# Kernel optimization log

Measured on AMD Instinct MI355X. Metric: run time of the kernel, lower is better.

Reference implementation:

```python
import jax, jax.numpy as jnp
import numpy as np

IMG_X, IMG_Y = 1333.0, 402.0   # image_size
MIN_SIZE = 16.0
NMS_THRESH = 0.7
PRE = 12000                    # n_train_pre_nms
POST = 2000                    # n_train_post_nms
HH, WW, A = 83, 25, 9          # 1333//16, 402//16, anchors per cell
N_ANCH = HH * WW * A           # 18675
B = 16


def setup_inputs() -> dict:
    key = jax.random.key(0)
    k1, k2, k3, k4, k5, k6 = jax.random.split(key, 6)
    # realistic anchor boxes inside the image
    xc = jax.random.uniform(k1, (N_ANCH,)) * IMG_X
    yc = jax.random.uniform(k2, (N_ANCH,)) * IMG_Y
    bw = jax.random.uniform(k3, (N_ANCH,)) * 240.0 + 16.0
    bh = jax.random.uniform(k4, (N_ANCH,)) * 120.0 + 16.0
    anchor_boxes = jnp.stack([xc - 0.5 * bw, yc - 0.5 * bh, xc + 0.5 * bw, yc + 0.5 * bh], axis=1)
    rpn_cls_score = jax.random.normal(k5, (B, N_ANCH * 2), dtype=jnp.float32)
    rpn_bbox_pred = jax.random.normal(k6, (B, N_ANCH, 4), dtype=jnp.float32) * 0.2
    return dict(anchor_boxes=anchor_boxes, rpn_cls_score=rpn_cls_score,
                rpn_bbox_pred=rpn_bbox_pred, rpn_cls_loss=jnp.zeros((1,), jnp.float32),
                rpn_bbox_loss=jnp.zeros((1,), jnp.float32))


def _decode(anchor_boxes, rpn_bbox_pred):
    ah = anchor_boxes[:, 3] - anchor_boxes[:, 1]
    aw = anchor_boxes[:, 2] - anchor_boxes[:, 0]
    acy = anchor_boxes[:, 1] + 0.5 * ah
    acx = anchor_boxes[:, 0] + 0.5 * aw
    dx = rpn_bbox_pred[..., 0]
    dy = rpn_bbox_pred[..., 1]
    dw = rpn_bbox_pred[..., 2]
    dh = rpn_bbox_pred[..., 3]
    cy = dy * ah + acy
    cx = dx * aw + acx
    h = jnp.exp(dh) * ah
    w = jnp.exp(dw) * aw
    # clip: x coords to [0, image_size[0]], y coords to [0, image_size[1]] (as in source)
    x1 = jnp.clip(cx - 0.5 * w, 0.0, IMG_X)
    y1 = jnp.clip(cy - 0.5 * h, 0.0, IMG_Y)
    x2 = jnp.clip(cx + 0.5 * w, 0.0, IMG_X)
    y2 = jnp.clip(cy + 0.5 * h, 0.0, IMG_Y)
    return jnp.stack([x1, y1, x2, y2], axis=-1)  # [N,4] broadcast over batch -> [B,N,4]


def _nms_one(roi, score):
    # roi: [N,4], score: [N]
    hs = roi[:, 3] - roi[:, 1]
    ws = roi[:, 2] - roi[:, 0]
    valid = (hs >= MIN_SIZE) & (ws >= MIN_SIZE)
    s = jnp.where(valid, score, -jnp.inf)
    idx = jnp.argsort(-s)[:PRE]          # score-descending, top pre_nms; invalid sink to end
    boxes = roi[idx]                      # score-sorted candidate boxes [PRE,4]
    vp = valid[idx]                       # which slots are real (passed size filter)
    # source quirk: order = order.argsort()[::-1] -> NMS visits boxes by DESCENDING
    # original-anchor-index; invalid slots get key -1 so they come last.
    seq_key = jnp.where(vp, idx, -1)
    perm = jnp.argsort(-seq_key)          # positions into score-sorted arrays, visit order
    x1, y1, x2, y2 = boxes[:, 0], boxes[:, 1], boxes[:, 2], boxes[:, 3]
    areas = (x2 - x1 + 1.0) * (y2 - y1 + 1.0)

    def step(alive, _):
        a_seq = alive[perm]
        any_alive = a_seq.any()
        j = perm[jnp.argmax(a_seq)]       # first surviving box in visit order
        xx1 = jnp.maximum(x1[j], x1)
        yy1 = jnp.maximum(y1[j], y1)
        xx2 = jnp.minimum(x2[j], x2)
        yy2 = jnp.minimum(y2[j], y2)
        inter = jnp.maximum(0.0, xx2 - xx1 + 1.0) * jnp.maximum(0.0, yy2 - yy1 + 1.0)
        ovr = inter / (areas[j] + areas - inter)
        alive = alive & jnp.where(any_alive, ovr <= NMS_THRESH, True)  # j kills itself (ovr=1)
        return alive, jnp.where(any_alive, j, -1)

    _, keep = jax.lax.scan(step, vp, None, length=POST)   # up to post_nms kept positions
    kmask = keep >= 0
    out = jnp.where(kmask[:, None], boxes[jnp.maximum(keep, 0)], 0.0)  # padded [POST,4]
    return out, kmask


def reference(anchor_boxes, rpn_cls_score, rpn_bbox_pred, rpn_cls_loss, rpn_bbox_loss):
    bsz = rpn_cls_score.shape[0]
    # objectness = view(B, 83, 25, 9, 2)[..., 1]
    score = rpn_cls_score.reshape(bsz, HH, WW, A, 2)[..., 1].reshape(bsz, -1)
    roi = _decode(anchor_boxes, rpn_bbox_pred)            # [B,N,4]
    rois, mask = jax.vmap(_nms_one)(roi, score)           # [B,POST,4], [B,POST]
    return rois, mask
```

## Files before the change

kernel.cpp:

```cpp
#include <hip/hip_runtime.h>
#include <math.h>

#define N_ANCHN 18675
#define NPAD    18688
#define BATCH   16
#define PRE     12000
#define CPAD    12032
#define WPB     188
#define POST    2000
#define NMS_T   0.7f
#define IMGX    1333.0f
#define IMGY    402.0f
#define MINSZ   16.0f
#define NBUCK   256
#define KINV    0x007FFFFFu
#define MLCAP   12288

typedef unsigned long long u64;

__device__ __forceinline__ unsigned key_of(float f) {
  unsigned u = __float_as_uint(f);
  return (u & 0x80000000u) ? ~u : (u | 0x80000000u);
}

__device__ __forceinline__ float iou_ref(float ax1, float ay1, float ax2, float ay2, float aar,
                                         float bx1, float by1, float bx2, float by2, float bar) {
  float xx1 = fmaxf(ax1, bx1);
  float yy1 = fmaxf(ay1, by1);
  float xx2 = fminf(ax2, bx2);
  float yy2 = fminf(ay2, by2);
  float iw = fmaxf(0.0f, __fadd_rn(__fsub_rn(xx2, xx1), 1.0f));
  float ih = fmaxf(0.0f, __fadd_rn(__fsub_rn(yy2, yy1), 1.0f));
  float inter = __fmul_rn(iw, ih);
  return __fdiv_rn(inter, __fsub_rn(__fadd_rn(aar, bar), inter));
}

__device__ __forceinline__ bool hit_test(float ix1, float iy1, float ix2, float iy2, float iar,
                                         float jx1, float jy1, float jx2, float jy2, float jar) {
  float xx1 = fmaxf(ix1, jx1);
  float yy1 = fmaxf(iy1, jy1);
  float xx2 = fminf(ix2, jx2);
  float yy2 = fminf(iy2, jy2);
  float iw = fmaxf(0.0f, __fadd_rn(__fsub_rn(xx2, xx1), 1.0f));
  float ih = fmaxf(0.0f, __fadd_rn(__fsub_rn(yy2, yy1), 1.0f));
  float inter = __fmul_rn(iw, ih);
  float S = __fadd_rn(iar, jar);
  if (inter >= __fmul_rn(0.43f, S)) return true;
  if (inter <= __fmul_rn(0.395f, S)) return false;
  return __fdiv_rn(inter, __fsub_rn(S, inter)) > NMS_T;
}

__device__ __forceinline__ void emit_hit(int lo, int hi, u64* diagb, unsigned* rcb,
                                         unsigned short* rtb, int L) {
  if ((hi >> 6) == (lo >> 6)) {
    atomicOr(&diagb[(size_t)(lo >> 6) * 64 + (lo & 63)], 1ull << (hi & 63));
  } else {
    unsigned slot = atomicAdd(&rcb[lo], 1u);
    if ((int)slot < L) rtb[(size_t)lo * L + slot] = (unsigned short)hi;
  }
}

__device__ __forceinline__ void decode_one(
    const float* __restrict__ anchors, const float* __restrict__ cls,
    const float* __restrict__ bbox, int b, int i,
    float& x1, float& y1, float& x2, float& y2, unsigned& key) {
  float4 A = *(const float4*)(anchors + (size_t)i * 4);
  float ah = __fsub_rn(A.w, A.y);
  float aw = __fsub_rn(A.z, A.x);
  float acy = __fadd_rn(A.y, __fmul_rn(0.5f, ah));
  float acx = __fadd_rn(A.x, __fmul_rn(0.5f, aw));

  float4 P = *(const float4*)(bbox + ((size_t)b * N_ANCHN + i) * 4);
  float dx = P.x, dy = P.y, dw = P.z, dh = P.w;

  float cy = __fadd_rn(__fmul_rn(dy, ah), acy);
  float cx = __fadd_rn(__fmul_rn(dx, aw), acx);
  float eh = (float)exp((double)dh);
  float ew = (float)exp((double)dw);
  float h = __fmul_rn(eh, ah);
  float w = __fmul_rn(ew, aw);

  x1 = fminf(fmaxf(__fsub_rn(cx, __fmul_rn(0.5f, w)), 0.0f), IMGX);
  y1 = fminf(fmaxf(__fsub_rn(cy, __fmul_rn(0.5f, h)), 0.0f), IMGY);
  x2 = fminf(fmaxf(__fadd_rn(cx, __fmul_rn(0.5f, w)), 0.0f), IMGX);
  y2 = fminf(fmaxf(__fadd_rn(cy, __fmul_rn(0.5f, h)), 0.0f), IMGY);

  bool valid = (__fsub_rn(y2, y1) >= MINSZ) && (__fsub_rn(x2, x1) >= MINSZ);
  float s = valid ? cls[(size_t)b * (2 * N_ANCHN) + 2 * i + 1] : -INFINITY;
  key = key_of(s);
}

__global__ __launch_bounds__(256) void decode_kernel(
    const float* __restrict__ anchors, const float* __restrict__ cls,
    const float* __restrict__ bbox,
    float* __restrict__ bx1, float* __restrict__ by1,
    float* __restrict__ bx2, float* __restrict__ by2,
    unsigned* __restrict__ keys,
    u64* __restrict__ diag, unsigned* __restrict__ rowcnt) {
  const int bx = blockIdx.x;
  const int b = blockIdx.y;
  if (bx == gridDim.x - 1) {
    u64* dz = diag + (size_t)b * WPB * 64;
    for (int i = threadIdx.x; i < WPB * 64; i += 256) dz[i] = 0ull;
    unsigned* rz = rowcnt + (size_t)b * CPAD;
    for (int i = threadIdx.x; i < CPAD; i += 256) rz[i] = 0u;
    return;
  }
  int i = bx * 256 + threadIdx.x;
  if (i >= N_ANCHN) return;
  float x1, y1, x2, y2; unsigned k;
  decode_one(anchors, cls, bbox, b, i, x1, y1, x2, y2, k);
  size_t o = (size_t)b * NPAD + i;
  bx1[o] = x1; by1[o] = y1; bx2[o] = x2; by2[o] = y2;
  keys[o] = k;
}

__global__ __launch_bounds__(1024) void prepsort_kernel(
    const unsigned* __restrict__ keys,
    const float* __restrict__ bx1, const float* __restrict__ by1,
    const float* __restrict__ bx2, const float* __restrict__ by2,
    float* __restrict__ cx1, float* __restrict__ cy1,
    float* __restrict__ cx2, float* __restrict__ cy2,
    float* __restrict__ car, int* __restrict__ ncand,
    float* __restrict__ sx1, float* __restrict__ sy1,
    float* __restrict__ sx2, float* __restrict__ sy2,
    float* __restrict__ sar, int* __restrict__ sperm,
    float* __restrict__ wminx1, float* __restrict__ wmaxx2) {
  const int b = blockIdx.x;
  const int tid = threadIdx.x;
  const int lane = tid & 63;
  const int wv = tid >> 6;
  __shared__ unsigned hist[16][256];
  __shared__ unsigned mh[256];
  __shared__ unsigned wsum[16];
  __shared__ unsigned bh[NBUCK];
  __shared__ unsigned boff[NBUCK];
  __shared__ unsigned char fb[NPAD];
  __shared__ unsigned short mlist[MLCAP];
  __shared__ unsigned sh_prefix, sh_k, sh_n, sh_mcount;
  const unsigned* kb = keys + (size_t)b * NPAD;

  if (tid == 0) { sh_prefix = 0u; sh_k = PRE; sh_mcount = 0u; }
  __syncthreads();

  {
    for (int idx = tid; idx < 16 * 256; idx += 1024) ((unsigned*)hist)[idx] = 0u;
    __syncthreads();
    for (int i = tid; i < N_ANCHN; i += 1024)
      atomicAdd(&hist[wv][kb[i] >> 24], 1u);
    __syncthreads();
    if (tid < 256) {
      unsigned s = 0;
#pragma unroll
      for (int q = 0; q < 16; ++q) s += hist[q][tid];
      mh[tid] = s;
    }
    __syncthreads();
    if (tid == 0) {
      unsigned kk = sh_k, cum = 0;
      for (int d = 255; d >= 0; --d) {
        unsigned c = mh[d];
        if (cum + c >= kk) { sh_k = kk - cum; sh_prefix = (unsigned)d << 24; break; }
        cum += c;
      }
    }
    __syncthreads();
  }

  {
    unsigned b0 = sh_prefix >> 24;
    for (int i = tid; i < N_ANCHN; i += 1024) {
      if ((kb[i] >> 24) == b0) {
        unsigned p = atomicAdd(&sh_mcount, 1u);
        if (p < MLCAP) mlist[p] = (unsigned short)i;
      }
    }
  }
  __syncthreads();
  const bool useList = (sh_mcount <= (unsigned)MLCAP);
  const unsigned mcount = min(sh_mcount, (unsigned)MLCAP);

  for (int level = 1; level < 4; ++level) {
    const int shift = 24 - 8 * level;
    for (int idx = tid; idx < 16 * 256; idx += 1024) ((unsigned*)hist)[idx] = 0u;
    __syncthreads();
    unsigned pre = sh_prefix;
    if (useList) {
      for (int idx = tid; idx < (int)mcount; idx += 1024) {
        unsigned k = kb[mlist[idx]];
        if ((k >> (shift + 8)) == (pre >> (shift + 8)))
          atomicAdd(&hist[wv][(k >> shift) & 255u], 1u);
      }
    } else {
      for (int i = tid; i < N_ANCHN; i += 1024) {
        unsigned k = kb[i];
        if ((k >> (shift + 8)) == (pre >> (shift + 8)))
          atomicAdd(&hist[wv][(k >> shift) & 255u], 1u);
      }
    }
    __syncthreads();
    if (tid < 256) {
      unsigned s = 0;
#pragma unroll
      for (int q = 0; q < 16; ++q) s += hist[q][tid];
      mh[tid] = s;
    }
    __syncthreads();
    if (tid == 0) {
      unsigned kk = sh_k, cum = 0;
      for (int d = 255; d >= 0; --d) {
        unsigned c = mh[d];
        if (cum + c >= kk) { sh_k = kk - cum; sh_prefix = pre | ((unsigned)d << shift); break; }
        cum += c;
      }
    }
    __syncthreads();
  }
  const unsigned T = sh_prefix;
  const unsigned slots = sh_k;

  const int SEG = (N_ANCHN + 1023) / 1024;

  {
    int i0 = tid * SEG, i1 = min(N_ANCHN, i0 + SEG);
    unsigned cnt = 0;
    for (int i = i0; i < i1; ++i) cnt += (kb[i] == T) ? 1u : 0u;
    unsigned v = cnt;
#pragma unroll
    for (int d = 1; d < 64; d <<= 1) {
      unsigned y = __shfl_up(v, d, 64);
      if (lane >= d) v += y;
    }
    if (lane == 63) wsum[wv] = v;
    __syncthreads();
    if (tid == 0) {
      unsigned acc = 0;
#pragma unroll
      for (int q = 0; q < 16; ++q) { unsigned t = wsum[q]; wsum[q] = acc; acc += t; }
    }
    __syncthreads();
    unsigned r = wsum[wv] + v - cnt;
    for (int i = i0; i < i1; ++i) {
      unsigned k = kb[i];
      bool tie = (k == T);
      bool cand = (k > T) || (tie && T > KINV && r < slots);
      if (tie) r++;
      fb[i] = cand ? (unsigned char)1 : (unsigned char)0;
    }
  }
  __syncthreads();

  const float* X1 = bx1 + (size_t)b * NPAD;
  const float* Y1 = by1 + (size_t)b * NPAD;
  const float* X2 = bx2 + (size_t)b * NPAD;
  const float* Y2 = by2 + (size_t)b * NPAD;
  {
    int j0 = tid * SEG, j1 = min(N_ANCHN, j0 + SEG);
    unsigned cnt = 0;
    for (int j = j0; j < j1; ++j) cnt += fb[N_ANCHN - 1 - j];
    unsigned v = cnt;
#pragma unroll
    for (int d = 1; d < 64; d <<= 1) {
      unsigned y = __shfl_up(v, d, 64);
      if (lane >= d) v += y;
    }
    if (lane == 63) wsum[wv] = v;
    __syncthreads();
    if (tid == 0) {
      unsigned acc = 0;
#pragma unroll
      for (int q = 0; q < 16; ++q) { unsigned t = wsum[q]; wsum[q] = acc; acc += t; }
      sh_n = acc;
    }
    __syncthreads();
    unsigned p = wsum[wv] + v - cnt;
    if (tid == 0) ncand[b] = (int)sh_n;
    float* CX1 = cx1 + (size_t)b * CPAD;
    float* CY1 = cy1 + (size_t)b * CPAD;
    float* CX2 = cx2 + (size_t)b * CPAD;
    float* CY2 = cy2 + (size_t)b * CPAD;
    float* CAR = car + (size_t)b * CPAD;
    for (int j = j0; j < j1; ++j) {
      int i = N_ANCHN - 1 - j;
      if (fb[i]) {
        float x1v = X1[i], y1v = Y1[i], x2v = X2[i], y2v = Y2[i];
        CX1[p] = x1v; CY1[p] = y1v; CX2[p] = x2v; CY2[p] = y2v;
        CAR[p] = __fmul_rn(__fadd_rn(__fsub_rn(x2v, x1v), 1.0f),
                           __fadd_rn(__fsub_rn(y2v, y1v), 1.0f));
        p++;
      }
    }
  }
  __syncthreads();
  const int n = (int)sh_n;

  const float scale = (float)NBUCK / 1334.0f;
  const float* CX1 = cx1 + (size_t)b * CPAD;
  const float* CY1 = cy1 + (size_t)b * CPAD;
  const float* CX2 = cx2 + (size_t)b * CPAD;
  const float* CY2 = cy2 + (size_t)b * CPAD;
  const float* CAR = car + (size_t)b * CPAD;
  float* SX1 = sx1 + (size_t)b * CPAD;
  float* SY1 = sy1 + (size_t)b * CPAD;
  float* SX2 = sx2 + (size_t)b * CPAD;
  float* SY2 = sy2 + (size_t)b * CPAD;
  float* SAR = sar + (size_t)b * CPAD;
  int* SP = sperm + (size_t)b * CPAD;

  if (tid < NBUCK) bh[tid] = 0u;
  __syncthreads();
  for (int i = tid; i < n; i += 1024) {
    int q = (int)(CX1[i] * scale);
    q = q < 0 ? 0 : (q > NBUCK - 1 ? NBUCK - 1 : q);
    atomicAdd(&bh[q], 1u);
  }
  __syncthreads();
  if (tid < 64) {
    unsigned carry = 0;
    for (int c = 0; c < 4; ++c) {
      unsigned own = bh[c * 64 + tid];
      unsigned v = own;
      for (int d = 1; d < 64; d <<= 1) {
        unsigned y = __shfl_up(v, d, 64);
        if (tid >= d) v += y;
      }
      boff[c * 64 + tid] = carry + v - own;
      carry += __shfl(v, 63, 64);
    }
  }
  __syncthreads();
  for (int i = tid; i < n; i += 1024) {
    float x1v = CX1[i];
    int q = (int)(x1v * scale);
    q = q < 0 ? 0 : (q > NBUCK - 1 ? NBUCK - 1 : q);
    unsigned p = atomicAdd(&boff[q], 1u);
    SX1[p] = x1v; SY1[p] = CY1[i]; SX2[p] = CX2[i]; SY2[p] = CY2[i];
    SAR[p] = CAR[i]; SP[p] = i;
  }
  for (int i = n + tid; i < CPAD; i += 1024) {
    SX1[i] = 1e30f; SY1[i] = 1e30f; SX2[i] = -1e30f; SY2[i] = -1e30f;
    SAR[i] = 1.0f; SP[i] = 0;
  }
  __syncthreads();
  for (int w = wv; w < WPB; w += 16) {
    float mn = SX1[64 * w + lane];
    float mx = SX2[64 * w + lane];
#pragma unroll
    for (int d = 32; d > 0; d >>= 1) {
      mn = fminf(mn, __shfl_xor(mn, d, 64));
      mx = fmaxf(mx, __shfl_xor(mx, d, 64));
    }
    if (lane == 0) {
      wminx1[(size_t)b * WPB + w] = mn;
      wmaxx2[(size_t)b * WPB + w] = mx;
    }
  }
}

__global__ __launch_bounds__(256) void build_kernel(
    const float* __restrict__ sx1, const float* __restrict__ sy1,
    const float* __restrict__ sx2, const float* __restrict__ sy2,
    const float* __restrict__ sar, const int* __restrict__ sperm,
    const int* __restrict__ ncand,
    const float* __restrict__ wminx1, const float* __restrict__ wmaxx2,
    u64* __restrict__ diagT, unsigned* __restrict__ rowcnt,
    unsigned short* __restrict__ rows_t, int L) {
  const int R = blockIdx.x, G0 = blockIdx.y, b = blockIdx.z;
  const int n = ncand[b];
  if (64 * R >= n) return;
  if (16 * G0 + 15 < R) return;
  const float* WMN = wminx1 + (size_t)b * WPB;
  const float rlim = __fadd_rn(wmaxx2[(size_t)b * WPB + R], 2.0f);
  {
    const int wlo = max(16 * G0, R);
    if (WMN[wlo] > __fadd_rn(rlim, 5.25f)) return;
  }

  const float* SX1 = sx1 + (size_t)b * CPAD;
  const float* SY1 = sy1 + (size_t)b * CPAD;
  const float* SX2 = sx2 + (size_t)b * CPAD;
  const float* SY2 = sy2 + (size_t)b * CPAD;
  const float* SAR = sar + (size_t)b * CPAD;
  const int* SP = sperm + (size_t)b * CPAD;

  const int t = threadIdx.x, lane = t & 63, q = t >> 6;

  __shared__ float4 rbv[64];
  __shared__ float2 ras[64];
  if (t < 64) {
    int i = 64 * R + t;
    rbv[t] = make_float4(SX1[i], SY1[i], SX2[i], SY2[i]);
  } else if (t < 128) {
    int i = 64 * R + (t - 64);
    ras[t - 64] = make_float2(SAR[i], __int_as_float(SP[i]));
  }
  const float rx2own = SX2[64 * R + lane];
  __syncthreads();

  const int w0 = 16 * G0 + 4 * q;
  const float wmn0 = WMN[min(w0 + 0, WPB - 1)];
  const float wmn1 = WMN[min(w0 + 1, WPB - 1)];
  const float wmn2 = WMN[min(w0 + 2, WPB - 1)];
  const float wmn3 = WMN[min(w0 + 3, WPB - 1)];
  const bool v0 = (w0 + 0 < WPB) && (w0 + 0 >= R) && (wmn0 <= rlim);
  const bool v1 = (w0 + 1 < WPB) && (w0 + 1 >= R) && (wmn1 <= rlim);
  const bool v2 = (w0 + 2 < WPB) && (w0 + 2 >= R) && (wmn2 <= rlim);
  const bool v3 = (w0 + 3 < WPB) && (w0 + 3 >= R) && (wmn3 <= rlim);
  if (!(v0 | v1 | v2 | v3)) return;

  float c0x1 = 1e30f, c0y1 = 0.f, c0x2 = 0.f, c0y2 = 0.f, c0ar = 1.f; int c0sp = 0;
  float c1x1 = 1e30f, c1y1 = 0.f, c1x2 = 0.f, c1y2 = 0.f, c1ar = 1.f; int c1sp = 0;
  float c2x1 = 1e30f, c2y1 = 0.f, c2x2 = 0.f, c2y2 = 0.f, c2ar = 1.f; int c2sp = 0;
  float c3x1 = 1e30f, c3y1 = 0.f, c3x2 = 0.f, c3y2 = 0.f, c3ar = 1.f; int c3sp = 0;
  if (v0) { int j = 64 * (w0 + 0) + lane;
    c0x1 = SX1[j]; c0y1 = SY1[j]; c0x2 = SX2[j]; c0y2 = SY2[j]; c0ar = SAR[j]; c0sp = SP[j]; }
  if (v1) { int j = 64 * (w0 + 1) + lane;
    c1x1 = SX1[j]; c1y1 = SY1[j]; c1x2 = SX2[j]; c1y2 = SY2[j]; c1ar = SAR[j]; c1sp = SP[j]; }
  if (v2) { int j = 64 * (w0 + 2) + lane;
    c2x1 = SX1[j]; c2y1 = SY1[j]; c2x2 = SX2[j]; c2y2 = SY2[j]; c2ar = SAR[j]; c2sp = SP[j]; }
  if (v3) { int j = 64 * (w0 + 3) + lane;
    c3x1 = SX1[j]; c3y1 = SY1[j]; c3x2 = SX2[j]; c3y2 = SY2[j]; c3ar = SAR[j]; c3sp = SP[j]; }

  const float wmnlo = v0 ? wmn0 : (v1 ? wmn1 : (v2 ? wmn2 : wmn3));
  u64 a = __ballot(rx2own >= __fsub_rn(wmnlo, 2.0f));
  if (!a) return;

  const float wmn0m2 = __fsub_rn(wmn0, 2.0f);
  const float wmn1m2 = __fsub_rn(wmn1, 2.0f);
  const float wmn2m2 = __fsub_rn(wmn2, 2.0f);
  const float wmn3m2 = __fsub_rn(wmn3, 2.0f);

  u64* diagb = diagT + (size_t)b * WPB * 64;
  unsigned* rcb = rowcnt + (size_t)b * CPAD;
  unsigned short* rtb = rows_t + (size_t)b * L * CPAD;

  const bool diagIn = (w0 <= R) & (R <= w0 + 3);
  if (!diagIn) {
    int k = (int)__builtin_ctzll(a);
    float4 RB = rbv[k];
    float2 AS = ras[k];
    while (true) {
      a &= a - 1;
      const int kn = a ? (int)__builtin_ctzll(a) : 0;
      const float4 RBn = rbv[kn];
      const float2 ASn = ras[kn];
      const float rx2k = RB.z;
      const float rark = AS.x;
      const int rsp = __float_as_int(AS.y);
      if (v0 && rx2k >= wmn0m2 &&
          hit_test(RB.x, RB.y, RB.z, RB.w, rark, c0x1, c0y1, c0x2, c0y2, c0ar))
        emit_hit(min(rsp, c0sp), max(rsp, c0sp), diagb, rcb, rtb, L);
      if (v1 && rx2k >= wmn1m2 &&
          hit_test(RB.x, RB.y, RB.z, RB.w, rark, c1x1, c1y1, c1x2, c1y2, c1ar))
        emit_hit(min(rsp, c1sp), max(rsp, c1sp), diagb, rcb, rtb, L);
      if (v2 && rx2k >= wmn2m2 &&
          hit_test(RB.x, RB.y, RB.z, RB.w, rark, c2x1, c2y1, c2x2, c2y2, c2ar))
        emit_hit(min(rsp, c2sp), max(rsp, c2sp), diagb, rcb, rtb, L);
      if (v3 && rx2k >= wmn3m2 &&
          hit_test(RB.x, RB.y, RB.z, RB.w, rark, c3x1, c3y1, c3x2, c3y2, c3ar))
        emit_hit(min(rsp, c3sp), max(rsp, c3sp), diagb, rcb, rtb, L);
      if (!a) break;
      RB = RBn; AS = ASn;
    }
  } else {
    const bool g0 = (w0 + 0 > R), e0 = (w0 + 0 == R);
    const bool g1 = (w0 + 1 > R), e1 = (w0 + 1 == R);
    const bool g2 = (w0 + 2 > R), e2 = (w0 + 2 == R);
    const bool g3 = (w0 + 3 > R), e3 = (w0 + 3 == R);
    int k = (int)__builtin_ctzll(a);
    float4 RB = rbv[k];
    float2 AS = ras[k];
    while (true) {
      a &= a - 1;
      const int kn = a ? (int)__builtin_ctzll(a) : 0;
      const float4 RBn = rbv[kn];
      const float2 ASn = ras[kn];
      const float rx2k = RB.z;
      const float rark = AS.x;
      const int rsp = __float_as_int(AS.y);
      if (v0 && rx2k >= wmn0m2) {
        bool dd = g0 | (e0 & (lane > k));
        if (dd && hit_test(RB.x, RB.y, RB.z, RB.w, rark, c0x1, c0y1, c0x2, c0y2, c0ar))
          emit_hit(min(rsp, c0sp), max(rsp, c0sp), diagb, rcb, rtb, L);
      }
      if (v1 && rx2k >= wmn1m2) {
        bool dd = g1 | (e1 & (lane > k));
        if (dd && hit_test(RB.x, RB.y, RB.z, RB.w, rark, c1x1, c1y1, c1x2, c1y2, c1ar))
          emit_hit(min(rsp, c1sp), max(rsp, c1sp), diagb, rcb, rtb, L);
      }
      if (v2 && rx2k >= wmn2m2) {
        bool dd = g2 | (e2 & (lane > k));
        if (dd && hit_test(RB.x, RB.y, RB.z, RB.w, rark, c2x1, c2y1, c2x2, c2y2, c2ar))
          emit_hit(min(rsp, c2sp), max(rsp, c2sp), diagb, rcb, rtb, L);
      }
      if (v3 && rx2k >= wmn3m2) {
        bool dd = g3 | (e3 & (lane > k));
        if (dd && hit_test(RB.x, RB.y, RB.z, RB.w, rark, c3x1, c3y1, c3x2, c3y2, c3ar))
          emit_hit(min(rsp, c3sp), max(rsp, c3sp), diagb, rcb, rtb, L);
      }
      if (!a) break;
      k = kn; RB = RBn; AS = ASn;
    }
  }
}

#define DECLW(s) u64 kw##s; unsigned cw##s; uint4 p0##s, p1##s;
#define LOADW(s, wexp) { int w_ = (wexp); int c_ = 64 * w_ + lane; \
  kw##s = diagb[(size_t)w_ * 64 + lane]; cw##s = rcb[c_]; \
  const uint4* rp_ = (const uint4*)(rtb + (size_t)c_ * L); p0##s = rp_[0]; p1##s = rp_[1]; }
#define PROCW(s, wexp) { int w_ = (wexp); \
  if (w_ < nw && sc < POST) { \
    const int base_ = 64 * w_; const int myc_ = base_ + lane; \
    const u64 suppw_ = supp[w_]; \
    const bool alv_ = (myc_ < n) && !((suppw_ >> lane) & 1ull); \
    u64 act_ = __ballot(alv_); \
    u64 selw_ = 0ull; \
    const int scb_ = sc; \
    const unsigned klo_ = (unsigned)kw##s, khi_ = (unsigned)(kw##s >> 32); \
    while (act_ && sc < POST) { \
      const int j_ = (int)__builtin_ctzll(act_); \
      const u64 kj_ = ((u64)(unsigned)__builtin_amdgcn_readlane((int)khi_, j_) << 32) | \
                      (u64)(unsigned)__builtin_amdgcn_readlane((int)klo_, j_); \
      selw_ |= 1ull << j_; sc++; \
      act_ &= ~(kj_ | (1ull << j_)); } \
    const bool selme_ = ((selw_ >> lane) & 1ull) != 0ull; \
    if (selme_) { \
      const int rank_ = scb_ + (int)__popcll(selw_ & ((1ull << lane) - 1ull)); \
      sel[rank_] = myc_; \
      const int ce_ = min((int)cw##s, L); \
      uint4 p2_ = {0,0,0,0}, p3_ = {0,0,0,0}; \
      if (ce_ > 16) { \
        const uint4* rp_ = (const uint4*)(rtb + (size_t)myc_ * L); \
        p2_ = rp_[2]; p3_ = rp_[3]; \
      } \
      unsigned ev_[8] = {p0##s.x, p0##s.y, p0##s.z, p0##s.w, p1##s.x, p1##s.y, p1##s.z, p1##s.w}; \
      _Pragma("unroll") \
      for (int u_ = 0; u_ < 8; ++u_) { \
        if (2 * u_ < ce_)     { int t_ = (int)(ev_[u_] & 0xffffu); atomicOr(&supp[t_ >> 6], 1ull << (t_ & 63)); } \
        if (2 * u_ + 1 < ce_) { int t_ = (int)(ev_[u_] >> 16);     atomicOr(&supp[t_ >> 6], 1ull << (t_ & 63)); } } \
      if (ce_ > 16) { \
        unsigned e2_[8] = {p2_.x, p2_.y, p2_.z, p2_.w, p3_.x, p3_.y, p3_.z, p3_.w}; \
        _Pragma("unroll") \
        for (int u_ = 0; u_ < 8; ++u_) { \
          if (16 + 2 * u_ < ce_)     { int t_ = (int)(e2_[u_] & 0xffffu); atomicOr(&supp[t_ >> 6], 1ull << (t_ & 63)); } \
          if (16 + 2 * u_ + 1 < ce_) { int t_ = (int)(e2_[u_] >> 16);     atomicOr(&supp[t_ >> 6], 1ull << (t_ & 63)); } } } } \
    u64 om_ = __ballot(selme_ && ((int)cw##s > L)); \
    while (om_) { \
      int j_ = (int)__builtin_ctzll(om_); om_ &= om_ - 1; \
      const int mc_ = base_ + j_; \
      float ax1_ = CX1[mc_], ay1_ = CY1[mc_], ax2_ = CX2[mc_], ay2_ = CY2[mc_], aar_ = CAR[mc_]; \
      for (int c2_ = base_ + 64 + lane; c2_ < n; c2_ += 64) { \
        float ovr_ = iou_ref(ax1_, ay1_, ax2_, ay2_, aar_, CX1[c2_], CY1[c2_], CX2[c2_], CY2[c2_], CAR[c2_]); \
        if (ovr_ > NMS_T) atomicOr(&supp[c2_ >> 6], 1ull << (c2_ & 63)); } } } }

#define LOADG(s, gexp) { int g_ = (gexp); \
  LOADW(s##0, min(4 * g_ + 0, WPB - 1)) \
  LOADW(s##1, min(4 * g_ + 1, WPB - 1)) \
  LOADW(s##2, min(4 * g_ + 2, WPB - 1)) \
  LOADW(s##3, min(4 * g_ + 3, WPB - 1)) }
#define PROCG(s, gexp) { int gg_ = (gexp); \
  PROCW(s##0, 4 * gg_ + 0) \
  PROCW(s##1, 4 * gg_ + 1) \
  PROCW(s##2, 4 * gg_ + 2) \
  PROCW(s##3, 4 * gg_ + 3) }

__global__ __launch_bounds__(64) void scan_kernel(
    const float* __restrict__ cx1, const float* __restrict__ cy1,
    const float* __restrict__ cx2, const float* __restrict__ cy2,
    const float* __restrict__ car, const int* __restrict__ ncand,
    const u64* __restrict__ diagT, const unsigned* __restrict__ rowcnt,
    const unsigned short* __restrict__ rows_t, int L,
    float* __restrict__ out) {
  const int b = blockIdx.x;
  const int lane = threadIdx.x;
  __shared__ u64 supp[WPB];
  __shared__ int sel[POST];
  for (int idx = lane; idx < WPB; idx += 64) supp[idx] = 0ull;

  const int n = ncand[b];
  const u64* diagb = diagT + (size_t)b * WPB * 64;
  const unsigned* rcb = rowcnt + (size_t)b * CPAD;
  const unsigned short* rtb = rows_t + (size_t)b * L * CPAD;
  const float* CX1 = cx1 + (size_t)b * CPAD;
  const float* CY1 = cy1 + (size_t)b * CPAD;
  const float* CX2 = cx2 + (size_t)b * CPAD;
  const float* CY2 = cy2 + (size_t)b * CPAD;
  const float* CAR = car + (size_t)b * CPAD;

  const int nw = (n + 63) >> 6;
  int sc = 0;

  DECLW(a0) DECLW(a1) DECLW(a2) DECLW(a3)
  DECLW(b0) DECLW(b1) DECLW(b2) DECLW(b3)
  DECLW(c0) DECLW(c1) DECLW(c2) DECLW(c3)

  if (nw > 0) {
    LOADG(a, 0)
    LOADG(b, 1)
    LOADG(c, 2)
    const int ng = (nw + 3) >> 2;
    for (int g = 0; g < ng && sc < POST; g += 3) {
      PROCG(a, g)
      LOADG(a, g + 3)
      PROCG(b, g + 1)
      LOADG(b, g + 4)
      PROCG(c, g + 2)
      LOADG(c, g + 5)
    }
  }

  float* roib = out + (size_t)b * POST * 4;
  float* maskb = out + (size_t)BATCH * POST * 4 + (size_t)b * POST;
  for (int t = lane; t < POST; t += 64) {
    if (t < sc) {
      int j = sel[t];
      float4 v = make_float4(CX1[j], CY1[j], CX2[j], CY2[j]);
      *(float4*)(roib + (size_t)t * 4) = v;
      maskb[t] = 1.0f;
    } else {
      *(float4*)(roib + (size_t)t * 4) = make_float4(0.f, 0.f, 0.f, 0.f);
      maskb[t] = 0.0f;
    }
  }
}

__global__ __launch_bounds__(256) void decode_fb_kernel(
    const float* __restrict__ anchors, const float* __restrict__ cls,
    const float* __restrict__ bbox,
    float* __restrict__ bx1, float* __restrict__ by1,
    float* __restrict__ bx2, float* __restrict__ by2,
    unsigned* __restrict__ keys) {
  int i = blockIdx.x * 256 + threadIdx.x;
  if (i >= N_ANCHN) return;
  int b = blockIdx.y;
  float x1, y1, x2, y2; unsigned k;
  decode_one(anchors, cls, bbox, b, i, x1, y1, x2, y2, k);
  size_t o = (size_t)b * NPAD + i;
  bx1[o] = x1; by1[o] = y1; bx2[o] = x2; by2[o] = y2;
  keys[o] = k;
}

__global__ __launch_bounds__(1024) void prep_kernel(
    const unsigned* __restrict__ keys,
    const float* __restrict__ bx1, const float* __restrict__ by1,
    const float* __restrict__ bx2, const float* __restrict__ by2,
    unsigned char* __restrict__ flags,
    float* __restrict__ cx1, float* __restrict__ cy1,
    float* __restrict__ cx2, float* __restrict__ cy2,
    float* __restrict__ car, int* __restrict__ ncand) {
  const int b = blockIdx.x;
  const int tid = threadIdx.x;
  __shared__ unsigned hist[256];
  __shared__ unsigned ssc[1024];
  __shared__ unsigned sh_prefix, sh_k;
  const unsigned* kb = keys + (size_t)b * NPAD;

  if (tid == 0) { sh_prefix = 0u; sh_k = PRE; }
  __syncthreads();

  for (int level = 0; level < 4; ++level) {
    const int shift = 24 - 8 * level;
    if (tid < 256) hist[tid] = 0u;
    __syncthreads();
    unsigned pre = sh_prefix;
    for (int i = tid; i < N_ANCHN; i += 1024) {
      unsigned k = kb[i];
      bool match = (level == 0) || ((k >> (shift + 8)) == (pre >> (shift + 8)));
      if (match) atomicAdd(&hist[(k >> shift) & 255u], 1u);
    }
    __syncthreads();
    if (tid == 0) {
      unsigned kk = sh_k, cum = 0;
      for (int d = 255; d >= 0; --d) {
        unsigned c = hist[d];
        if (cum + c >= kk) { sh_k = kk - cum; sh_prefix = pre | ((unsigned)d << shift); break; }
        cum += c;
      }
    }
    __syncthreads();
  }
  const unsigned T = sh_prefix;

  unsigned local = 0;
  for (int i = tid; i < N_ANCHN; i += 1024) local += (kb[i] > T) ? 1u : 0u;
  ssc[tid] = local;
  __syncthreads();
  for (int off = 512; off > 0; off >>= 1) {
    if (tid < off) ssc[tid] += ssc[tid + off];
    __syncthreads();
  }
  const unsigned slots = PRE - ssc[0];
  __syncthreads();

  const int SEG = (N_ANCHN + 1023) / 1024;
  const float* X1 = bx1 + (size_t)b * NPAD;
  const float* Y1 = by1 + (size_t)b * NPAD;
  const float* X2 = bx2 + (size_t)b * NPAD;
  const float* Y2 = by2 + (size_t)b * NPAD;
  unsigned char* fb = flags + (size_t)b * NPAD;

  {
    int i0 = tid * SEG, i1 = min(N_ANCHN, i0 + SEG);
    unsigned cnt = 0;
    for (int i = i0; i < i1; ++i) cnt += (kb[i] == T) ? 1u : 0u;
    ssc[tid] = cnt;
    __syncthreads();
    for (int off = 1; off < 1024; off <<= 1) {
      unsigned v = (tid >= off) ? ssc[tid - off] : 0u;
      __syncthreads();
      ssc[tid] += v;
      __syncthreads();
    }
    unsigned r = ssc[tid] - cnt;
    for (int i = i0; i < i1; ++i) {
      unsigned k = kb[i];
      bool valid = (__fsub_rn(Y2[i], Y1[i]) >= MINSZ) && (__fsub_rn(X2[i], X1[i]) >= MINSZ);
      bool tie = (k == T);
      bool cand = valid && ((k > T) || (tie && r < slots));
      if (tie) r++;
      fb[i] = cand ? (unsigned char)1 : (unsigned char)0;
    }
  }
  __syncthreads();

  {
    int j0 = tid * SEG, j1 = min(N_ANCHN, j0 + SEG);
    unsigned cnt = 0;
    for (int j = j0; j < j1; ++j) cnt += fb[N_ANCHN - 1 - j];
    ssc[tid] = cnt;
    __syncthreads();
    for (int off = 1; off < 1024; off <<= 1) {
      unsigned v = (tid >= off) ? ssc[tid - off] : 0u;
      __syncthreads();
      ssc[tid] += v;
      __syncthreads();
    }
    unsigned p = ssc[tid] - cnt;
    if (tid == 0) ncand[b] = (int)ssc[1023];
    float* CX1 = cx1 + (size_t)b * CPAD;
    float* CY1 = cy1 + (size_t)b * CPAD;
    float* CX2 = cx2 + (size_t)b * CPAD;
    float* CY2 = cy2 + (size_t)b * CPAD;
    float* CAR = car + (size_t)b * CPAD;
    for (int j = j0; j < j1; ++j) {
      int i = N_ANCHN - 1 - j;
      if (fb[i]) {
        float x1v = X1[i], y1v = Y1[i], x2v = X2[i], y2v = Y2[i];
        CX1[p] = x1v; CY1[p] = y1v; CX2[p] = x2v; CY2[p] = y2v;
        CAR[p] = __fmul_rn(__fadd_rn(__fsub_rn(x2v, x1v), 1.0f),
                           __fadd_rn(__fsub_rn(y2v, y1v), 1.0f));
        p++;
      }
    }
  }
}

__global__ __launch_bounds__(1024) void nms_kernel(
    const float* __restrict__ cx1, const float* __restrict__ cy1,
    const float* __restrict__ cx2, const float* __restrict__ cy2,
    const float* __restrict__ car, const int* __restrict__ ncand,
    float* __restrict__ out) {
  const int b = blockIdx.x;
  const int tid = threadIdx.x;
  __shared__ float sx1[POST], sy1[POST], sx2[POST], sy2[POST], sar[POST];
  __shared__ int Lbuf[1024];
  __shared__ int wcount[16];
  __shared__ int sh_sc;

  const float* CX1 = cx1 + (size_t)b * CPAD;
  const float* CY1 = cy1 + (size_t)b * CPAD;
  const float* CX2 = cx2 + (size_t)b * CPAD;
  const float* CY2 = cy2 + (size_t)b * CPAD;
  const float* CAR = car + (size_t)b * CPAD;
  float* roib = out + (size_t)b * POST * 4;
  float* maskb = out + (size_t)BATCH * POST * 4 + (size_t)b * POST;

  const int n = ncand[b];
  if (tid == 0) sh_sc = 0;
  __syncthreads();
  const int lane = tid & 63;
  const int w = tid >> 6;

  for (int base = 0; base < n; base += 1024) {
    const int c = base + tid;
    bool pass = (c < n);
    float px1 = 0, py1 = 0, px2 = 0, py2 = 0, par = 0;
    if (pass) { px1 = CX1[c]; py1 = CY1[c]; px2 = CX2[c]; py2 = CY2[c]; par = CAR[c]; }
    const int sc0 = sh_sc;

    if (pass) {
      for (int k = 0; k < sc0; ++k) {
        float ovr = iou_ref(sx1[k], sy1[k], sx2[k], sy2[k], sar[k], px1, py1, px2, py2, par);
        if (ovr > NMS_T) { pass = false; break; }
      }
    }

    unsigned long long bal = __ballot(pass);
    if (lane == 0) wcount[w] = (int)__popcll(bal);
    __syncthreads();
    int off = 0;
    for (int q = 0; q < 16; ++q) off += (q < w) ? wcount[q] : 0;
    if (pass) Lbuf[off + (int)__popcll(bal & ((1ULL << lane) - 1ULL))] = c;
    __syncthreads();

    if (tid < 64) {
      int total = 0;
      for (int q = 0; q < 16; ++q) total += wcount[q];
      int sc = sc0;
      for (int g = 0; g < total && sc < POST; g += 64) {
        int idx = (g + lane < total) ? Lbuf[g + lane] : -1;
        float qx1 = 0, qy1 = 0, qx2 = 0, qy2 = 0, qar = 0;
        bool al = (idx >= 0);
        if (al) { qx1 = CX1[idx]; qy1 = CY1[idx]; qx2 = CX2[idx]; qy2 = CY2[idx]; qar = CAR[idx]; }
        for (int k = sc0; k < sc && al; ++k) {
          float ovr = iou_ref(sx1[k], sy1[k], sx2[k], sy2[k], sar[k], qx1, qy1, qx2, qy2, qar);
          if (ovr > NMS_T) al = false;
        }
        unsigned long long alive = __ballot(al);
        while (alive && sc < POST) {
          int j = (int)__builtin_ctzll(alive);
          float jx1 = __shfl(qx1, j), jy1 = __shfl(qy1, j);
          float jx2 = __shfl(qx2, j), jy2 = __shfl(qy2, j), jar = __shfl(qar, j);
          float ovr = iou_ref(jx1, jy1, jx2, jy2, jar, qx1, qy1, qx2, qy2, qar);
          unsigned long long killm = __ballot(ovr > NMS_T);
          alive &= ~killm;
          alive &= ~(1ULL << j);
          if (lane == 0) {
            sx1[sc] = jx1; sy1[sc] = jy1; sx2[sc] = jx2; sy2[sc] = jy2; sar[sc] = jar;
            roib[(size_t)sc * 4 + 0] = jx1;
            roib[(size_t)sc * 4 + 1] = jy1;
            roib[(size_t)sc * 4 + 2] = jx2;
            roib[(size_t)sc * 4 + 3] = jy2;
          }
          sc++;
        }
      }
      if (lane == 0) sh_sc = sc;
    }
    __syncthreads();
    if (sh_sc >= POST) break;
  }
  __syncthreads();

  const int sc = sh_sc;
  for (int t = tid; t < POST; t += 1024) {
    if (t >= sc) {
      roib[(size_t)t * 4 + 0] = 0.f; roib[(size_t)t * 4 + 1] = 0.f;
      roib[(size_t)t * 4 + 2] = 0.f; roib[(size_t)t * 4 + 3] = 0.f;
    }
    maskb[t] = (t < sc) ? 1.0f : 0.0f;
  }
}

extern "C" void kernel_launch(void* const* d_in, const int* in_sizes, int n_in,
                              void* d_out, int out_size, void* d_ws, size_t ws_size,
                              hipStream_t stream) {
  const float* anchors = (const float*)d_in[0];
  const float* cls = (const float*)d_in[1];
  const float* bbox = (const float*)d_in[2];
  float* out = (float*)d_out;
  char* ws = (char*)d_ws;

  size_t o = 0;
  float* cx1 = (float*)(ws + o); o += (size_t)BATCH * CPAD * 4;
  float* cy1 = (float*)(ws + o); o += (size_t)BATCH * CPAD * 4;
  float* cx2 = (float*)(ws + o); o += (size_t)BATCH * CPAD * 4;
  float* cy2 = (float*)(ws + o); o += (size_t)BATCH * CPAD * 4;
  float* car = (float*)(ws + o); o += (size_t)BATCH * CPAD * 4;
  int* ncand = (int*)(ws + o); o += 256;
  u64* diag = (u64*)(ws + o); o += (size_t)BATCH * WPB * 64 * 8;
  unsigned* rowcnt = (unsigned*)(ws + o); o += (size_t)BATCH * CPAD * 4;
  float* wminx1 = (float*)(ws + o); o += (size_t)BATCH * WPB * 4;
  float* wmaxx2 = (float*)(ws + o); o += (size_t)BATCH * WPB * 4;
  float* sx1 = (float*)(ws + o); o += (size_t)BATCH * CPAD * 4;
  float* sy1 = (float*)(ws + o); o += (size_t)BATCH * CPAD * 4;
  float* sx2 = (float*)(ws + o); o += (size_t)BATCH * CPAD * 4;
  float* sy2 = (float*)(ws + o); o += (size_t)BATCH * CPAD * 4;
  float* sar = (float*)(ws + o); o += (size_t)BATCH * CPAD * 4;
  int* sperm = (int*)(ws + o); o += (size_t)BATCH * CPAD * 4;
  size_t overlay = o;
  unsigned* keys = (unsigned*)(ws + overlay);
  float* bx1 = (float*)(ws + overlay + (size_t)BATCH * NPAD * 4 * 1);
  float* by1 = (float*)(ws + overlay + (size_t)BATCH * NPAD * 4 * 2);
  float* bx2 = (float*)(ws + overlay + (size_t)BATCH * NPAD * 4 * 3);
  float* by2 = (float*)(ws + overlay + (size_t)BATCH * NPAD * 4 * 4);
  size_t decode_bytes = (size_t)BATCH * NPAD * 4 * 5;
  unsigned short* rows_t = (unsigned short*)(ws + overlay);

  int L = 0;
  for (int Ltry = 32; Ltry >= 16; Ltry -= 16) {
    size_t rows_bytes = (size_t)BATCH * Ltry * CPAD * 2;
    size_t need = overlay + (decode_bytes > rows_bytes ? decode_bytes : rows_bytes);
    if (ws_size >= need) { L = Ltry; break; }
  }

  if (L > 0) {
    dim3 dgrid((N_ANCHN + 255) / 256 + 1, BATCH);
    decode_kernel<<<dgrid, 256, 0, stream>>>(anchors, cls, bbox, bx1, by1, bx2, by2,
                                             keys, diag, rowcnt);
    prepsort_kernel<<<BATCH, 1024, 0, stream>>>(keys, bx1, by1, bx2, by2,
                                                cx1, cy1, cx2, cy2, car, ncand,
                                                sx1, sy1, sx2, sy2, sar, sperm,
                                                wminx1, wmaxx2);
    build_kernel<<<dim3(WPB, (WPB + 15) / 16, BATCH), 256, 0, stream>>>(
        sx1, sy1, sx2, sy2, sar, sperm, ncand, wminx1, wmaxx2,
        diag, rowcnt, rows_t, L);
    scan_kernel<<<BATCH, 64, 0, stream>>>(cx1, cy1, cx2, cy2, car, ncand,
                                          diag, rowcnt, rows_t, L, out);
  } else {
    size_t f = 0;
    unsigned* fkeys = (unsigned*)(ws + f); f += (size_t)BATCH * NPAD * 4;
    float* fbx1 = (float*)(ws + f); f += (size_t)BATCH * NPAD * 4;
    float* fby1 = (float*)(ws + f); f += (size_t)BATCH * NPAD * 4;
    float* fbx2 = (float*)(ws + f); f += (size_t)BATCH * NPAD * 4;
    float* fby2 = (float*)(ws + f); f += (size_t)BATCH * NPAD * 4;
    float* fcx1 = (float*)(ws + f); f += (size_t)BATCH * CPAD * 4;
    float* fcy1 = (float*)(ws + f); f += (size_t)BATCH * CPAD * 4;
    float* fcx2 = (float*)(ws + f); f += (size_t)BATCH * CPAD * 4;
    float* fcy2 = (float*)(ws + f); f += (size_t)BATCH * CPAD * 4;
    float* fcar = (float*)(ws + f); f += (size_t)BATCH * CPAD * 4;
    unsigned char* fflags = (unsigned char*)(ws + f); f += (size_t)BATCH * NPAD;
    int* fncand = (int*)(ws + f); f += 256;

    dim3 dgrid((N_ANCHN + 255) / 256, BATCH);
    decode_fb_kernel<<<dgrid, 256, 0, stream>>>(anchors, cls, bbox, fbx1, fby1, fbx2, fby2, fkeys);
    prep_kernel<<<BATCH, 1024, 0, stream>>>(fkeys, fbx1, fby1, fbx2, fby2, fflags,
                                            fcx1, fcy1, fcx2, fcy2, fcar, fncand);
    nms_kernel<<<BATCH, 1024, 0, stream>>>(fcx1, fcy1, fcx2, fcy2, fcar, fncand, out);
  }
}
```

Before: 530.1 us.

## Use x-sorted window pruning for overflow rows and allow larger per-row lists

In the scan kernel, a selected box whose suppression list overflows the stored row length no longer compares against every later candidate by brute force. It walks the x-sorted candidate copy and uses per-word min/max x bounds to skip or stop early, then maps hits back through the permutation. The stored row length can now reach 64 entries, with a tail loop reading entries past 32, so fewer rows overflow. In exchange this uses more workspace and memory traffic for the row table, and adds some serial per-entry atomics.

```diff
diff --git a/kernel.cpp b/kernel.cpp
--- a/kernel.cpp
+++ b/kernel.cpp
@@ -543,15 +543,25 @@
         _Pragma("unroll") \
         for (int u_ = 0; u_ < 8; ++u_) { \
           if (16 + 2 * u_ < ce_)     { int t_ = (int)(e2_[u_] & 0xffffu); atomicOr(&supp[t_ >> 6], 1ull << (t_ & 63)); } \
-          if (16 + 2 * u_ + 1 < ce_) { int t_ = (int)(e2_[u_] >> 16);     atomicOr(&supp[t_ >> 6], 1ull << (t_ & 63)); } } } } \
+          if (16 + 2 * u_ + 1 < ce_) { int t_ = (int)(e2_[u_] >> 16);     atomicOr(&supp[t_ >> 6], 1ull << (t_ & 63)); } } } \
+      for (int e_ = 32; e_ < ce_; ++e_) { \
+        int t_ = (int)rtb[(size_t)myc_ * L + e_]; atomicOr(&supp[t_ >> 6], 1ull << (t_ & 63)); } } \
     u64 om_ = __ballot(selme_ && ((int)cw##s > L)); \
     while (om_) { \
       int j_ = (int)__builtin_ctzll(om_); om_ &= om_ - 1; \
       const int mc_ = base_ + j_; \
       float ax1_ = CX1[mc_], ay1_ = CY1[mc_], ax2_ = CX2[mc_], ay2_ = CY2[mc_], aar_ = CAR[mc_]; \
-      for (int c2_ = base_ + 64 + lane; c2_ < n; c2_ += 64) { \
-        float ovr_ = iou_ref(ax1_, ay1_, ax2_, ay2_, aar_, CX1[c2_], CY1[c2_], CX2[c2_], CY2[c2_], CAR[c2_]); \
-        if (ovr_ > NMS_T) atomicOr(&supp[c2_ >> 6], 1ull << (c2_ & 63)); } } } }
+      const float xhi_ = __fadd_rn(ax2_, 2.0f); \
+      const float xlo_ = __fsub_rn(ax1_, 2.0f); \
+      for (int w2_ = 0; w2_ < nw; ++w2_) { \
+        if (WMN[w2_] > xhi_) break; \
+        if (WMX[w2_] < xlo_) continue; \
+        int sj_ = 64 * w2_ + lane; \
+        float ovr_ = iou_ref(ax1_, ay1_, ax2_, ay2_, aar_, \
+                             SX1[sj_], SY1[sj_], SX2[sj_], SY2[sj_], SAR[sj_]); \
+        if (ovr_ > NMS_T) { \
+          int cj_ = SP[sj_]; \
+          if (cj_ >= base_ + 64) atomicOr(&supp[cj_ >> 6], 1ull << (cj_ & 63)); } } } } }
 
 #define LOADG(s, gexp) { int g_ = (gexp); \
   LOADW(s##0, min(4 * g_ + 0, WPB - 1)) \
@@ -568,6 +578,10 @@
     const float* __restrict__ cx1, const float* __restrict__ cy1,
     const float* __restrict__ cx2, const float* __restrict__ cy2,
     const float* __restrict__ car, const int* __restrict__ ncand,
+    const float* __restrict__ sx1, const float* __restrict__ sy1,
+    const float* __restrict__ sx2, const float* __restrict__ sy2,
+    const float* __restrict__ sar, const int* __restrict__ sperm,
+    const float* __restrict__ wminx1, const float* __restrict__ wmaxx2,
     const u64* __restrict__ diagT, const unsigned* __restrict__ rowcnt,
     const unsigned short* __restrict__ rows_t, int L,
     float* __restrict__ out) {
@@ -586,6 +600,14 @@
   const float* CX2 = cx2 + (size_t)b * CPAD;
   const float* CY2 = cy2 + (size_t)b * CPAD;
   const float* CAR = car + (size_t)b * CPAD;
+  const float* SX1 = sx1 + (size_t)b * CPAD;
+  const float* SY1 = sy1 + (size_t)b * CPAD;
+  const float* SX2 = sx2 + (size_t)b * CPAD;
+  const float* SY2 = sy2 + (size_t)b * CPAD;
+  const float* SAR = sar + (size_t)b * CPAD;
+  const int* SP = sperm + (size_t)b * CPAD;
+  const float* WMN = wminx1 + (size_t)b * WPB;
+  const float* WMX = wmaxx2 + (size_t)b * WPB;
 
   const int nw = (n + 63) >> 6;
   int sc = 0;
@@ -888,7 +910,7 @@
   unsigned short* rows_t = (unsigned short*)(ws + overlay);
 
   int L = 0;
-  for (int Ltry = 32; Ltry >= 16; Ltry -= 16) {
+  for (int Ltry = 64; Ltry >= 16; Ltry >>= 1) {
     size_t rows_bytes = (size_t)BATCH * Ltry * CPAD * 2;
     size_t need = overlay + (decode_bytes > rows_bytes ? decode_bytes : rows_bytes);
     if (ws_size >= need) { L = Ltry; break; }
@@ -906,6 +928,8 @@
         sx1, sy1, sx2, sy2, sar, sperm, ncand, wminx1, wmaxx2,
         diag, rowcnt, rows_t, L);
     scan_kernel<<<BATCH, 64, 0, stream>>>(cx1, cy1, cx2, cy2, car, ncand,
+                                          sx1, sy1, sx2, sy2, sar, sperm,
+                                          wminx1, wmaxx2,
                                           diag, rowcnt, rows_t, L, out);
   } else {
     size_t f = 0;
```

New measurement: 533.1 us. About the same (+0.6%).
